# Performance work log

Hardware: AMD Instinct MI355X
Metric: run time of the kernel (lower is better)

The kernel has to match this reference:

```python
import jax, jax.numpy as jnp
import numpy as np

NEG = -1e30  # finite stand-in for -inf (grad-safe)
GAMMA = 2.0
ALPHA = 1.0


def setup_inputs() -> dict:
    key = jax.random.key(0)
    k1, k2, k3 = jax.random.split(key, 3)
    N, T, C, S = 128, 64, 6625, 25
    logits = jax.random.normal(k1, (N, T, C), dtype=jnp.float32)
    # labels exclude blank (=0)
    targets = jax.random.randint(k2, (N, S), 1, C)
    target_length = jax.random.randint(k3, (N,), 1, S + 1)
    return {"logits": logits, "targets": targets, "target_length": target_length}


def _ctc_nll(log_probs, targets, lengths):
    """log_probs: [N,T,C] (already log-softmaxed). Returns per-sample NLL [N]."""
    N, T, C = log_probs.shape
    S = targets.shape[1]
    S_ext = 2 * S + 1
    # extended label sequence: blank, l1, blank, l2, ..., blank  -> [N, S_ext]
    ext = jnp.zeros((N, S_ext), dtype=targets.dtype).at[:, 1::2].set(targets)
    # gather extended-label log-probs -> [T, N, S_ext]
    idx = jnp.broadcast_to(ext[:, None, :], (N, T, S_ext))
    lp_ext = jnp.transpose(jnp.take_along_axis(log_probs, idx, axis=2), (1, 0, 2))
    # skip transition s-2 -> s allowed iff ext[s] != blank and ext[s] != ext[s-2]
    ext_m2 = jnp.pad(ext[:, :-2], ((0, 0), (2, 0)), constant_values=-1)
    can_skip = (ext != 0) & (ext != ext_m2)  # [N, S_ext]

    alpha0 = (jnp.full((N, S_ext), NEG, dtype=log_probs.dtype)
              .at[:, 0].set(lp_ext[0, :, 0])
              .at[:, 1].set(lp_ext[0, :, 1]))

    def step(alpha, lp_t):
        a1 = alpha
        a2 = jnp.pad(alpha[:, :-1], ((0, 0), (1, 0)), constant_values=NEG)
        a3 = jnp.where(can_skip,
                       jnp.pad(alpha[:, :-2], ((0, 0), (2, 0)), constant_values=NEG),
                       NEG)
        new = jnp.logaddexp(jnp.logaddexp(a1, a2), a3) + lp_t
        return new, None

    alphaT, _ = jax.lax.scan(step, alpha0, lp_ext[1:])
    L = jnp.clip(lengths, 1, T)  # module clamps target_length to [1, T]
    rows = jnp.arange(N)
    ll = jnp.logaddexp(alphaT[rows, 2 * L - 1], alphaT[rows, 2 * L])
    return -ll


def reference(logits, targets, target_length):
    x = jax.nn.log_softmax(logits, axis=2)           # [N,T,C]
    loss = _ctc_nll(x, targets, target_length)        # [N]
    weight = (1.0 - jnp.exp(-loss)) ** GAMMA          # focal reweighting
    loss = loss * weight * ALPHA
    return jnp.mean(loss)
```

## Files before the change

### kernel.cpp

```cpp
#include <hip/hip_runtime.h>
#include <hip/hip_bf16.h>
#include <stdint.h>

#define NN 128
#define TT 64
#define CC 6625
#define SS 25
#define SE 51
#define LPW 26
#define NEGV (-1e30f)

__global__ __launch_bounds__(256) void lse_gather_kernel(
    const float* __restrict__ logits,
    const int*   __restrict__ targets,
    float*       __restrict__ lp)
{
    const int row = blockIdx.x;
    const int tid = threadIdx.x;
    const float* __restrict__ x = logits + (size_t)row * CC;

    const int mis  = (int)(((uintptr_t)x) & 15u) >> 2;
    const int head = (4 - mis) & 3;
    const int nvec = (CC - head) >> 2;
    const int tail = head + (nvec << 2);

    float m0 = NEGV, m1 = NEGV, m2 = NEGV, m3 = NEGV;
    float s0 = 0.f,  s1 = 0.f,  s2 = 0.f,  s3 = 0.f;

#define UPD(mm, ss, vv)                              \
    do {                                             \
        float _v = (vv);                             \
        if (_v > mm) {                               \
            ss = ss * __expf(mm - _v) + 1.f;         \
            mm = _v;                                 \
        } else {                                     \
            ss += __expf(_v - mm);                   \
        }                                            \
    } while (0)

    for (int i = tid; i < head; i += 256) UPD(m0, s0, x[i]);
    const float4* __restrict__ xv = reinterpret_cast<const float4*>(x + head);
    for (int i = tid; i < nvec; i += 256) {
        float4 v = xv[i];
        UPD(m0, s0, v.x);
        UPD(m1, s1, v.y);
        UPD(m2, s2, v.z);
        UPD(m3, s3, v.w);
    }
    for (int i = tail + tid; i < CC; i += 256) UPD(m0, s0, x[i]);

    float m = fmaxf(fmaxf(m0, m1), fmaxf(m2, m3));
    float s = s0 * __expf(m0 - m) + s1 * __expf(m1 - m) +
              s2 * __expf(m2 - m) + s3 * __expf(m3 - m);

    for (int off = 1; off < 64; off <<= 1) {
        float om = __shfl_xor(m, off, 64);
        float os = __shfl_xor(s, off, 64);
        float nm = fmaxf(m, om);
        s = s * __expf(m - nm) + os * __expf(om - nm);
        m = nm;
    }

    __shared__ float sm[4], ssv[4];
    __shared__ float lse_sh;
    const int wid = tid >> 6;
    if ((tid & 63) == 0) { sm[wid] = m; ssv[wid] = s; }
    __syncthreads();
    if (tid == 0) {
        float M = sm[0], SSum = ssv[0];
        for (int w = 1; w < 4; ++w) {
            float nm = fmaxf(M, sm[w]);
            SSum = SSum * __expf(M - nm) + ssv[w] * __expf(sm[w] - nm);
            M = nm;
        }
        lse_sh = M + __logf(SSum);
    }
    __syncthreads();
    const float lse = lse_sh;

    if (tid < LPW) {
        const int n   = row / TT;
        const int cls = (tid == 0) ? 0 : targets[n * SS + tid - 1];
        lp[(size_t)row * LPW + tid] = x[cls] - lse;
    }
#undef UPD
}

__global__ __launch_bounds__(64) void ctc_alpha_kernel(
    const float* __restrict__ lp,
    const int*   __restrict__ targets,
    const int*   __restrict__ target_length,
    float*       __restrict__ sample_loss)
{
    const int n = blockIdx.x;
    const int s = threadIdx.x;
    const bool active = (s < SE);

    const int pos = (s & 1) ? (1 + (s >> 1)) : 0;

    bool can_skip = false;
    if (active && (s & 1)) {
        if (s == 1) can_skip = true;
        else {
            const int lab  = targets[n * SS + (s >> 1)];
            const int lab2 = targets[n * SS + (s >> 1) - 1];
            can_skip = (lab != lab2);
        }
    }

    const float* __restrict__ lpn = lp + (size_t)n * TT * LPW;

    float alpha = NEGV;
    {
        const float lp0 = active ? lpn[pos] : NEGV;
        if (s < 2) alpha = lp0;
    }

    for (int t = 1; t < TT; ++t) {
        const float a1 = alpha;
        float a2 = __shfl_up(alpha, 1, 64);
        if (s == 0) a2 = NEGV;
        float a3 = __shfl_up(alpha, 2, 64);
        if (s < 2 || !can_skip) a3 = NEGV;
        const float mx  = fmaxf(a1, fmaxf(a2, a3));
        const float sum = __expf(a1 - mx) + __expf(a2 - mx) + __expf(a3 - mx);
        const float lpt = active ? lpn[t * LPW + pos] : NEGV;
        float na = mx + __logf(sum) + lpt;
        alpha = active ? na : NEGV;
    }

    int L = target_length[n];
    L = (L < 1) ? 1 : ((L > SS) ? SS : L);
    const float aL1 = __shfl(alpha, 2 * L - 1, 64);
    const float aL2 = __shfl(alpha, 2 * L,     64);
    if (s == 0) {
        const float mx = fmaxf(aL1, aL2);
        const float ll = mx + __logf(__expf(aL1 - mx) + __expf(aL2 - mx));
        const float loss = -ll;
        const float w = 1.f - __expf(-loss);
        sample_loss[n] = loss * w * w;
    }
}

__global__ __launch_bounds__(128) void reduce_kernel(
    const float* __restrict__ sample_loss, float* __restrict__ out)
{
    float v = sample_loss[threadIdx.x];
    for (int off = 1; off < 64; off <<= 1) v += __shfl_xor(v, off, 64);
    __shared__ float tmp[2];
    if ((threadIdx.x & 63) == 0) tmp[threadIdx.x >> 6] = v;
    __syncthreads();
    if (threadIdx.x == 0) out[0] = (tmp[0] + tmp[1]) * (1.0f / NN);
}

extern "C" void kernel_launch(void* const* d_in, const int* in_sizes, int n_in,
                              void* d_out, int out_size, void* d_ws, size_t ws_size,
                              hipStream_t stream)
{
    const float* logits  = (const float*)d_in[0];
    const int*   targets = (const int*)  d_in[1];
    const int*   tlen    = (const int*)  d_in[2];
    float*       out     = (float*)d_out;

    float* lp          = (float*)d_ws;
    float* sample_loss = lp + (size_t)NN * TT * LPW;

    lse_gather_kernel<<<NN * TT, 256, 0, stream>>>(logits, targets, lp);
    ctc_alpha_kernel<<<NN, 64, 0, stream>>>(lp, targets, tlen, sample_loss);
    reduce_kernel<<<1, 128, 0, stream>>>(sample_loss, out);
}
```

Measured before the change: 319.7 us.

## Use two-pass register-resident softmax, prefetch CTC log-probs, fuse final reduction via atomics

The LSE kernel now loads each row's 6625 logits into registers up front (7 float4 per thread). It computes the global max first, then a plain sum of exponentials, which removes the branchy online-softmax rescaling and the per-element divergence. The CTC alpha kernel prefetches all 64 timesteps of gathered log-probs into registers before the recurrence, so the serial loop no longer stalls on memory. The separate reduce kernel is replaced by a memset plus an atomicAdd of each sample's scaled loss. This adds register pressure and makes the summation order nondeterministic.

```diff
diff --git a/kernel.cpp b/kernel.cpp
--- a/kernel.cpp
+++ b/kernel.cpp
@@ -24,73 +24,60 @@
     const int nvec = (CC - head) >> 2;
     const int tail = head + (nvec << 2);
 
-    float m0 = NEGV, m1 = NEGV, m2 = NEGV, m3 = NEGV;
-    float s0 = 0.f,  s1 = 0.f,  s2 = 0.f,  s3 = 0.f;
+    const float4* __restrict__ xv = reinterpret_cast<const float4*>(x + head);
 
-#define UPD(mm, ss, vv)                              \
-    do {                                             \
-        float _v = (vv);                             \
-        if (_v > mm) {                               \
-            ss = ss * __expf(mm - _v) + 1.f;         \
-            mm = _v;                                 \
-        } else {                                     \
-            ss += __expf(_v - mm);                   \
-        }                                            \
-    } while (0)
+    float4 v[7];
+#pragma unroll
+    for (int k = 0; k < 7; ++k) {
+        const int i = tid + (k << 8);
+        if (i < nvec) v[k] = xv[i];
+        else          v[k] = make_float4(NEGV, NEGV, NEGV, NEGV);
+    }
+    const float e0 = (tid < head)       ? x[tid]        : NEGV;
+    const float e1 = (tail + tid < CC)  ? x[tail + tid] : NEGV;
 
-    for (int i = tid; i < head; i += 256) UPD(m0, s0, x[i]);
-    const float4* __restrict__ xv = reinterpret_cast<const float4*>(x + head);
-    for (int i = tid; i < nvec; i += 256) {
-        float4 v = xv[i];
-        UPD(m0, s0, v.x);
-        UPD(m1, s1, v.y);
-        UPD(m2, s2, v.z);
-        UPD(m3, s3, v.w);
+    float m = fmaxf(e0, e1);
+#pragma unroll
+    for (int k = 0; k < 7; ++k) {
+        m = fmaxf(m, fmaxf(fmaxf(v[k].x, v[k].y), fmaxf(v[k].z, v[k].w)));
     }
-    for (int i = tail + tid; i < CC; i += 256) UPD(m0, s0, x[i]);
+#pragma unroll
+    for (int off = 1; off < 64; off <<= 1)
+        m = fmaxf(m, __shfl_xor(m, off, 64));
 
-    float m = fmaxf(fmaxf(m0, m1), fmaxf(m2, m3));
-    float s = s0 * __expf(m0 - m) + s1 * __expf(m1 - m) +
-              s2 * __expf(m2 - m) + s3 * __expf(m3 - m);
+    __shared__ float sm[4];
+    __shared__ float ssv[4];
+    const int wid = tid >> 6;
+    if ((tid & 63) == 0) sm[wid] = m;
+    __syncthreads();
+    const float M = fmaxf(fmaxf(sm[0], sm[1]), fmaxf(sm[2], sm[3]));
 
-    for (int off = 1; off < 64; off <<= 1) {
-        float om = __shfl_xor(m, off, 64);
-        float os = __shfl_xor(s, off, 64);
-        float nm = fmaxf(m, om);
-        s = s * __expf(m - nm) + os * __expf(om - nm);
-        m = nm;
+    float s = __expf(e0 - M) + __expf(e1 - M);
+#pragma unroll
+    for (int k = 0; k < 7; ++k) {
+        s += __expf(v[k].x - M) + __expf(v[k].y - M) +
+             __expf(v[k].z - M) + __expf(v[k].w - M);
     }
-
-    __shared__ float sm[4], ssv[4];
-    __shared__ float lse_sh;
-    const int wid = tid >> 6;
-    if ((tid & 63) == 0) { sm[wid] = m; ssv[wid] = s; }
+#pragma unroll
+    for (int off = 1; off < 64; off <<= 1)
+        s += __shfl_xor(s, off, 64);
+    if ((tid & 63) == 0) ssv[wid] = s;
     __syncthreads();
-    if (tid == 0) {
-        float M = sm[0], SSum = ssv[0];
-        for (int w = 1; w < 4; ++w) {
-            float nm = fmaxf(M, sm[w]);
-            SSum = SSum * __expf(M - nm) + ssv[w] * __expf(sm[w] - nm);
-            M = nm;
-        }
-        lse_sh = M + __logf(SSum);
-    }
-    __syncthreads();
-    const float lse = lse_sh;
+    const float S   = ssv[0] + ssv[1] + ssv[2] + ssv[3];
+    const float lse = M + __logf(S);
 
     if (tid < LPW) {
         const int n   = row / TT;
         const int cls = (tid == 0) ? 0 : targets[n * SS + tid - 1];
         lp[(size_t)row * LPW + tid] = x[cls] - lse;
     }
-#undef UPD
 }
 
 __global__ __launch_bounds__(64) void ctc_alpha_kernel(
     const float* __restrict__ lp,
     const int*   __restrict__ targets,
     const int*   __restrict__ target_length,
-    float*       __restrict__ sample_loss)
+    float*       __restrict__ out)
 {
     const int n = blockIdx.x;
     const int s = threadIdx.x;
@@ -110,12 +97,14 @@
 
     const float* __restrict__ lpn = lp + (size_t)n * TT * LPW;
 
-    float alpha = NEGV;
-    {
-        const float lp0 = active ? lpn[pos] : NEGV;
-        if (s < 2) alpha = lp0;
-    }
+    float lpt[TT];
+#pragma unroll
+    for (int t = 0; t < TT; ++t)
+        lpt[t] = active ? lpn[t * LPW + pos] : NEGV;
 
+    float alpha = (s < 2) ? lpt[0] : NEGV;
+
+#pragma unroll
     for (int t = 1; t < TT; ++t) {
         const float a1 = alpha;
         float a2 = __shfl_up(alpha, 1, 64);
@@ -124,9 +113,7 @@
         if (s < 2 || !can_skip) a3 = NEGV;
         const float mx  = fmaxf(a1, fmaxf(a2, a3));
         const float sum = __expf(a1 - mx) + __expf(a2 - mx) + __expf(a3 - mx);
-        const float lpt = active ? lpn[t * LPW + pos] : NEGV;
-        float na = mx + __logf(sum) + lpt;
-        alpha = active ? na : NEGV;
+        alpha = active ? (mx + __logf(sum) + lpt[t]) : NEGV;
     }
 
     int L = target_length[n];
@@ -138,19 +125,8 @@
         const float ll = mx + __logf(__expf(aL1 - mx) + __expf(aL2 - mx));
         const float loss = -ll;
         const float w = 1.f - __expf(-loss);
-        sample_loss[n] = loss * w * w;
+        atomicAdd(out, loss * w * w * (1.0f / NN));
     }
-}
-
-__global__ __launch_bounds__(128) void reduce_kernel(
-    const float* __restrict__ sample_loss, float* __restrict__ out)
-{
-    float v = sample_loss[threadIdx.x];
-    for (int off = 1; off < 64; off <<= 1) v += __shfl_xor(v, off, 64);
-    __shared__ float tmp[2];
-    if ((threadIdx.x & 63) == 0) tmp[threadIdx.x >> 6] = v;
-    __syncthreads();
-    if (threadIdx.x == 0) out[0] = (tmp[0] + tmp[1]) * (1.0f / NN);
 }
 
 extern "C" void kernel_launch(void* const* d_in, const int* in_sizes, int n_in,
@@ -162,10 +138,9 @@
     const int*   tlen    = (const int*)  d_in[2];
     float*       out     = (float*)d_out;
 
-    float* lp          = (float*)d_ws;
-    float* sample_loss = lp + (size_t)NN * TT * LPW;
+    float* lp = (float*)d_ws;
 
+    hipMemsetAsync(out, 0, sizeof(float) * out_size, stream);
     lse_gather_kernel<<<NN * TT, 256, 0, stream>>>(logits, targets, lp);
-    ctc_alpha_kernel<<<NN, 64, 0, stream>>>(lp, targets, tlen, sample_loss);
-    reduce_kernel<<<1, 128, 0, stream>>>(sample_loss, out);
+    ctc_alpha_kernel<<<NN, 64, 0, stream>>>(lp, targets, tlen, out);
 }
```

After: 307.5 us. 3.8% less time.
